# Kernel tuning notes

Hardware: AMD Instinct MI355X
Metric: run time of the kernel (lower is better)

## Reference

```python
import jax, jax.numpy as jnp
import numpy as np

LN_EPS = 1e-5
L1_EPS = 1e-12  # F.normalize clamp_min eps


def _layernorm(h, g, b):
    mu = h.mean(-1, keepdims=True)
    var = ((h - mu) ** 2).mean(-1, keepdims=True)
    return (h - mu) * jax.lax.rsqrt(var + LN_EPS) * g + b


def _graph(x, wq_w, wq_b, wk_w, wk_b, gcn_w, ln_g, ln_b):
    # x: [..., n, d]
    qx = x @ wq_w.T + wq_b
    kx = x @ wk_w.T + wk_b
    dot = jnp.einsum('...nd,...md->...nm', qx, kx)
    sq = dot * dot
    adj = sq / jnp.maximum(sq.sum(-1, keepdims=True), L1_EPS)  # L1-normalized rows
    for i in range(gcn_w.shape[0]):
        h = adj @ (x @ gcn_w[i])
        x = jax.nn.relu(_layernorm(h, ln_g[i], ln_b[i]))
    return x.mean(-2)  # mean over nodes -> [..., d]


def setup_inputs() -> dict:
    key = jax.random.key(0)
    ks = jax.random.split(key, 12)
    N, FR, B, NF = 16, 32, 50, 768
    L, NC = 2, 400
    s = 1.0 / np.sqrt(NF)
    inp = {
        'feats': jax.random.normal(ks[0], (N, FR, B, NF), jnp.float32),
        'feat_global_single': jax.random.normal(ks[1], (N, NF), jnp.float32),
        'feat_single_previous': jax.random.normal(ks[2], (N, NF), jnp.float32),
        'wq_w': jax.random.normal(ks[3], (NF, NF), jnp.float32) * s,
        'wq_b': jnp.zeros((NF,), jnp.float32),
        'wk_w': jax.random.normal(ks[4], (NF, NF), jnp.float32) * s,
        'wk_b': jnp.zeros((NF,), jnp.float32),
        'gcn_w': jax.random.normal(ks[5], (L, NF, NF), jnp.float32) * s,
        'ln_g': jnp.ones((L, NF), jnp.float32),
        'ln_b': jnp.zeros((L, NF), jnp.float32),
        'fc1_w': jax.random.normal(ks[6], (NF, 2 * NF), jnp.float32) / np.sqrt(2 * NF),
        'fc1_b': jnp.zeros((NF,), jnp.float32),
        'fc2_w': jax.random.normal(ks[7], (NC, NF), jnp.float32) * s,
        'fc2_b': jnp.zeros((NC,), jnp.float32),
        't_c': 0,
    }
    return inp


def reference(feats, feat_global_single, feat_single_previous,
              wq_w, wq_b, wk_w, wk_b, gcn_w, ln_g, ln_b,
              fc1_w, fc1_b, fc2_w, fc2_b, t_c):
    N, FR, B, NF = feats.shape
    x = feats.reshape(N * FR, B, NF)
    # object-level graph (shared weights)
    x = _graph(x, wq_w, wq_b, wk_w, wk_b, gcn_w, ln_g, ln_b)  # [N*FR, NF]
    x = x.reshape(N, FR, NF)
    # frame-level graph (same shared weights)
    x = _graph(x, wq_w, wq_b, wk_w, wk_b, gcn_w, ln_g, ln_b)  # [N, NF]
    y = jnp.concatenate([x, feat_global_single], axis=-1)      # [N, 2*NF]
    # ClassifierSimple (dropout = identity in eval)
    h = jax.nn.relu(y @ fc1_w.T + fc1_b)
    logits = h @ fc2_w.T + fc2_b
    return (logits, y)
```

## Files before the change

kernel.cpp:

```cpp
#include <hip/hip_runtime.h>
#include <hip/hip_bf16.h>

typedef unsigned short u16;
typedef unsigned int   u32;
typedef __attribute__((ext_vector_type(8))) short short8;
typedef __attribute__((ext_vector_type(4))) float float4v;

__device__ __forceinline__ float bf2f(u16 u){ union{u32 i; float f;} c; c.i = ((u32)u) << 16; return c.f; }
__device__ __forceinline__ float bflo(u32 u){ union{u32 i; float f;} c; c.i = u << 16; return c.f; }
__device__ __forceinline__ float bfhi(u32 u){ union{u32 i; float f;} c; c.i = u & 0xFFFF0000u; return c.f; }
__device__ __forceinline__ u16 f2bf(float f){
  union{float f; u32 i;} c; c.f = f; u32 x = c.i;
  return (u16)((x + 0x7FFFu + ((x >> 16) & 1u)) >> 16);
}
__device__ __forceinline__ u32 pack2(float a, float b){
  union { __hip_bfloat162 h; u32 u; } c;
  c.h = __float22bfloat162_rn(float2{a, b});
  return c.u;
}

__device__ __forceinline__ void async16(const void* g, void* l){
  __builtin_amdgcn_global_load_lds((const __attribute__((address_space(1))) void*)g,
                                   (__attribute__((address_space(3))) void*)l, 16, 0, 0);
}

__global__ void __launch_bounds__(256) conv_bf16(const float* __restrict__ src, u16* __restrict__ dst, int n8)
{
  int t = blockIdx.x * 256 + threadIdx.x;
  int stride = gridDim.x * 256;
  for (int i = t; i < n8; i += stride) {
    float4 a = ((const float4*)src)[2 * i];
    float4 b = ((const float4*)src)[2 * i + 1];
    uint4 o = { pack2(a.x, a.y), pack2(a.z, a.w), pack2(b.x, b.y), pack2(b.z, b.w) };
    ((uint4*)dst)[i] = o;
  }
}

__global__ void prep_qkw(const float* __restrict__ wq, const float* __restrict__ wk,
                         const float* __restrict__ wqb, const float* __restrict__ wkb,
                         u16* __restrict__ QHB, float* __restrict__ biasQH)
{
  int t = blockIdx.x * 256 + threadIdx.x;
  int stride = gridDim.x * 256;
  for (int i = t; i < 294912; i += stride) {
    float4 v = (i < 147456) ? ((const float4*)wq)[i] : ((const float4*)wk)[i - 147456];
    ushort4 o; o.x = f2bf(v.x); o.y = f2bf(v.y); o.z = f2bf(v.z); o.w = f2bf(v.w);
    ((ushort4*)QHB)[i] = o;
  }
  if (t < 768) biasQH[t] = wqb[t];
  else if (t < 1536) biasQH[t] = wkb[t - 768];
  else if (t < 2304) biasQH[t] = 0.f;
}

__global__ void prep_gcnT(const float* __restrict__ gcn, u16* __restrict__ QHB, u16* __restrict__ gcnT1)
{
  __shared__ float tile[32][33];
  int l = blockIdx.z;
  int d0 = blockIdx.y * 32, o0 = blockIdx.x * 32;
  int tx = threadIdx.x, ty = threadIdx.y;
  const float* src = gcn + (size_t)l * 589824;
  u16* dst = (l == 0) ? (QHB + (size_t)1536 * 768) : gcnT1;
  for (int i = 0; i < 32; i += 8) tile[ty + i][tx] = src[(size_t)(d0 + ty + i) * 768 + o0 + tx];
  __syncthreads();
  for (int i = 0; i < 32; i += 8) dst[(size_t)(o0 + ty + i) * 768 + d0 + tx] = f2bf(tile[tx][ty + i]);
}

__global__ void __launch_bounds__(256) gemm_bt(const u16* __restrict__ A, const u16* __restrict__ Bw,
                                               const float* __restrict__ bias, u16* __restrict__ C,
                                               int M, int N, int K)
{
  __shared__ __attribute__((aligned(16))) u16 As[128 * 64];
  __shared__ __attribute__((aligned(16))) u16 Bs[128 * 64];
  int tid = threadIdx.x, lane = tid & 63, wid = tid >> 6;
  int wm = wid >> 1, wn = wid & 1;
  size_t m0 = (size_t)blockIdx.x * 128, n0 = (size_t)blockIdx.y * 128;

  float4v acc[4][4];
  for (int r = 0; r < 4; r++) for (int c = 0; c < 4; c++) acc[r][c] = (float4v){0.f, 0.f, 0.f, 0.f};

  int srow8  = lane >> 3;
  int schunk = (lane & 7) ^ srow8;
  const u16* gA[4]; const u16* gB[4];
  u16* lA[4]; u16* lB[4];
#pragma unroll
  for (int j = 0; j < 4; j++) {
    int r = 32 * wid + 8 * j + srow8;
    gA[j] = A  + (m0 + r) * (size_t)K + schunk * 8;
    gB[j] = Bw + (n0 + r) * (size_t)K + schunk * 8;
    lA[j] = &As[(32 * wid + 8 * j) * 64];
    lB[j] = &Bs[(32 * wid + 8 * j) * 64];
  }

  int l15 = lane & 15, quad = lane >> 4;
  int s0 = quad ^ (l15 & 7);

  for (int kt = 0; kt < K; kt += 64) {
#pragma unroll
    for (int j = 0; j < 4; j++) {
      async16(gA[j] + kt, lA[j]);
      async16(gB[j] + kt, lB[j]);
    }
    __syncthreads();
#pragma unroll
    for (int ks = 0; ks < 2; ks++) {
      int so = (s0 ^ (ks << 2)) * 8;
      short8 af[4], bfr[4];
#pragma unroll
      for (int r = 0; r < 4; r++) af[r]  = *(const short8*)&As[(wm * 64 + r * 16 + l15) * 64 + so];
#pragma unroll
      for (int c = 0; c < 4; c++) bfr[c] = *(const short8*)&Bs[(wn * 64 + c * 16 + l15) * 64 + so];
#pragma unroll
      for (int r = 0; r < 4; r++)
#pragma unroll
        for (int c = 0; c < 4; c++)
          acc[r][c] = __builtin_amdgcn_mfma_f32_16x16x32_bf16(af[r], bfr[c], acc[r][c], 0, 0, 0);
    }
    __syncthreads();
  }

  int quad4 = quad * 4;
  for (int c = 0; c < 4; c++) {
    int n = (int)n0 + wn * 64 + c * 16 + l15;
    float bv = bias ? bias[n] : 0.f;
    for (int r = 0; r < 4; r++) {
      size_t mbase = m0 + wm * 64 + r * 16 + quad4;
      for (int t = 0; t < 4; t++)
        C[(mbase + t) * (size_t)N + n] = f2bf(acc[r][c][t] + bv);
    }
  }
}


template<int NP>
__global__ void __launch_bounds__(512) fused_l1(const u16* __restrict__ QH,
                                                const float* __restrict__ lng, const float* __restrict__ lnb,
                                                u16* __restrict__ adjG, u16* __restrict__ X, int n)
{
  constexpr int ST = 72;
  constexpr int TPW = (NP == 64) ? 2 : 1;
  __shared__ __attribute__((aligned(16))) u16 adjb[NP * ST];
  __shared__ __attribute__((aligned(16))) u16 HT[2][64 * ST];
  __shared__ float rsum[NP];
  __shared__ float stats[NP][2];
  __shared__ float bc[NP][2];
  __shared__ float lg[768], lb[768];

  int g = blockIdx.x;
  int tid = threadIdx.x, lane = tid & 63, w = tid >> 6;
  int l15 = lane & 15, quad = lane >> 4;

  for (int i = tid; i < 768; i += 512) { lg[i] = lng[i]; lb[i] = lnb[i]; }
  if (tid < NP) { rsum[tid] = 0.f; stats[tid][0] = 0.f; stats[tid][1] = 0.f; }
  __syncthreads();

  int mt, nt0; bool s_act;
  if (NP == 64) { mt = w & 3; nt0 = (w >> 2) * 2; s_act = true; }
  else          { mt = w & 1; nt0 = w >> 1;       s_act = (w < 4); }

  int rowA = mt * 16 + l15;
  bool aok = rowA < n;
  const u16* pA  = QH + ((size_t)g * n + rowA) * 2304 + quad * 8;
  int rowB0 = (nt0) * 16 + l15, rowB1 = (nt0 + TPW - 1) * 16 + l15;
  bool b0ok = rowB0 < n, b1ok = rowB1 < n;
  const u16* pB0 = QH + ((size_t)g * n + rowB0) * 2304 + 768 + quad * 8;
  const u16* pB1 = QH + ((size_t)g * n + rowB1) * 2304 + 768 + quad * 8;

  float4v sacc[TPW];
  for (int j = 0; j < TPW; j++) sacc[j] = (float4v){0.f, 0.f, 0.f, 0.f};

  if (s_act) {
    for (int kt = 0; kt < 768; kt += 32) {
      uint4 av = {0,0,0,0}, bv0 = {0,0,0,0}, bv1 = {0,0,0,0};
      if (aok)  av  = *(const uint4*)(pA + kt);
      if (b0ok) bv0 = *(const uint4*)(pB0 + kt);
      if (TPW == 2 && b1ok) bv1 = *(const uint4*)(pB1 + kt);
      short8 a = *(short8*)&av;
      sacc[0] = __builtin_amdgcn_mfma_f32_16x16x32_bf16(a, *(short8*)&bv0, sacc[0], 0, 0, 0);
      if (TPW == 2)
        sacc[1] = __builtin_amdgcn_mfma_f32_16x16x32_bf16(a, *(short8*)&bv1, sacc[1], 0, 0, 0);
    }
    for (int t = 0; t < 4; t++) {
      float s = 0.f;
      for (int j = 0; j < TPW; j++) { float v = sacc[j][t]; s += v * v; }
      s += __shfl_xor(s, 1); s += __shfl_xor(s, 2); s += __shfl_xor(s, 4); s += __shfl_xor(s, 8);
      if (l15 == 0) atomicAdd(&rsum[mt * 16 + quad * 4 + t], s);
    }
  }
  __syncthreads();
  if (tid < NP) rsum[tid] = 1.0f / fmaxf(rsum[tid], 1e-12f);
  __syncthreads();
  if (s_act) {
    u16* gadj = adjG + (size_t)g * NP * NP;
    for (int j = 0; j < TPW; j++)
      for (int t = 0; t < 4; t++) {
        int row = mt * 16 + quad * 4 + t, col = (nt0 + j) * 16 + l15;
        float v = sacc[j][t];
        u16 b = f2bf(v * v * rsum[row]);
        adjb[row * ST + col] = b;
        gadj[row * NP + col] = b;
      }
  }
  __syncthreads();

  int m2, nt20;
  if (NP == 64) { m2 = w & 3; nt20 = (w >> 2) * 2; }
  else          { m2 = w & 1; nt20 = w >> 1; }

  float4v xacc[12][TPW];
#pragma unroll
  for (int ch = 0; ch < 12; ch++) for (int j = 0; j < TPW; j++) xacc[ch][j] = (float4v){0.f,0.f,0.f,0.f};

  int hj  = tid & (NP - 1);
  int hseg= (NP == 64) ? w : ((tid >> 5) & 7);
  bool hact = (NP == 64) ? true : (tid < NP * 8);
  const u16* hbase = QH + ((size_t)g * n + hj) * 2304 + 1536 + hseg * 8;

  uint4 hcur = {0,0,0,0};
  if (hact && hj < n) hcur = *(const uint4*)(hbase);

#pragma unroll
  for (int ch = 0; ch < 12; ch++) {
    uint4 hnext = {0,0,0,0};
    if (ch < 11 && hact && hj < n) hnext = *(const uint4*)(hbase + (ch + 1) * 64);
    u16* htb = HT[ch & 1];
    if (hact) {
      const u16* ep = (const u16*)&hcur;
      for (int i = 0; i < 8; i++) htb[(hseg * 8 + i) * ST + hj] = ep[i];
    }
    __syncthreads();
    for (int k = 0; k < NP / 32; k++) {
      short8 a = *(const short8*)&adjb[(m2 * 16 + l15) * ST + k * 32 + quad * 8];
      for (int j = 0; j < TPW; j++) {
        short8 b = *(const short8*)&htb[((nt20 + j) * 16 + l15) * ST + k * 32 + quad * 8];
        xacc[ch][j] = __builtin_amdgcn_mfma_f32_16x16x32_bf16(a, b, xacc[ch][j], 0, 0, 0);
      }
    }
    hcur = hnext;
  }

  float ssum[4] = {0,0,0,0}, ssq[4] = {0,0,0,0};
#pragma unroll
  for (int ch = 0; ch < 12; ch++)
    for (int j = 0; j < TPW; j++)
      for (int t = 0; t < 4; t++) { float v = xacc[ch][j][t]; ssum[t] += v; ssq[t] += v * v; }
  for (int m = 1; m <= 8; m <<= 1)
    for (int t = 0; t < 4; t++) { ssum[t] += __shfl_xor(ssum[t], m); ssq[t] += __shfl_xor(ssq[t], m); }
  if (l15 == 0)
    for (int t = 0; t < 4; t++) {
      atomicAdd(&stats[m2 * 16 + quad * 4 + t][0], ssum[t]);
      atomicAdd(&stats[m2 * 16 + quad * 4 + t][1], ssq[t]);
    }
  __syncthreads();
  if (tid < NP) {
    float mu = stats[tid][0] * (1.f / 768.f);
    float var = stats[tid][1] * (1.f / 768.f) - mu * mu;
    bc[tid][0] = mu; bc[tid][1] = rsqrtf(fmaxf(var, 0.f) + 1e-5f);
  }
  __syncthreads();

#pragma unroll
  for (int ch = 0; ch < 12; ch++)
    for (int j = 0; j < TPW; j++)
      for (int t = 0; t < 4; t++) {
        int row = m2 * 16 + quad * 4 + t;
        if (row < n) {
          int d = ch * 64 + (nt20 + j) * 16 + l15;
          float v = fmaxf((xacc[ch][j][t] - bc[row][0]) * bc[row][1] * lg[d] + lb[d], 0.f);
          X[((size_t)g * n + row) * 768 + d] = f2bf(v);
        }
      }
}

template<int NP>
__global__ void __launch_bounds__(512) fused_l2(const u16* __restrict__ adjG, const u16* __restrict__ H,
                                                const float* __restrict__ lng, const float* __restrict__ lnb,
                                                u16* __restrict__ Xmean, int n, float inv)
{
  constexpr int ST = 72;
  constexpr int TPW = (NP == 64) ? 2 : 1;
  __shared__ __attribute__((aligned(16))) u16 adjb[NP * ST];
  __shared__ __attribute__((aligned(16))) u16 HT[2][64 * ST];
  __shared__ float stats[NP][2];
  __shared__ float bc[NP][2];
  __shared__ float colsum[768];
  __shared__ float lg[768], lb[768];

  int g = blockIdx.x;
  int tid = threadIdx.x, lane = tid & 63, w = tid >> 6;
  int l15 = lane & 15, quad = lane >> 4;

  for (int i = tid; i < 768; i += 512) { lg[i] = lng[i]; lb[i] = lnb[i]; colsum[i] = 0.f; }
  if (tid < NP) { stats[tid][0] = 0.f; stats[tid][1] = 0.f; }
  if (tid * 8 < NP * NP) {
    int row = (tid * 8) / NP, c0 = (tid * 8) % NP;
    uint4 v = *(const uint4*)(adjG + (size_t)g * NP * NP + row * NP + c0);
    *(uint4*)&adjb[row * ST + c0] = v;
  }

  int m2, nt20;
  if (NP == 64) { m2 = w & 3; nt20 = (w >> 2) * 2; }
  else          { m2 = w & 1; nt20 = w >> 1; }

  float4v xacc[12][TPW];
#pragma unroll
  for (int ch = 0; ch < 12; ch++) for (int j = 0; j < TPW; j++) xacc[ch][j] = (float4v){0.f,0.f,0.f,0.f};

  int hj  = tid & (NP - 1);
  int hseg= (NP == 64) ? w : ((tid >> 5) & 7);
  bool hact = (NP == 64) ? true : (tid < NP * 8);
  const u16* hbase = H + ((size_t)g * n + hj) * 768 + hseg * 8;

  uint4 hcur = {0,0,0,0};
  if (hact && hj < n) hcur = *(const uint4*)(hbase);

  __syncthreads();

#pragma unroll
  for (int ch = 0; ch < 12; ch++) {
    uint4 hnext = {0,0,0,0};
    if (ch < 11 && hact && hj < n) hnext = *(const uint4*)(hbase + (ch + 1) * 64);
    u16* htb = HT[ch & 1];
    if (hact) {
      const u16* ep = (const u16*)&hcur;
      for (int i = 0; i < 8; i++) htb[(hseg * 8 + i) * ST + hj] = ep[i];
    }
    __syncthreads();
    for (int k = 0; k < NP / 32; k++) {
      short8 a = *(const short8*)&adjb[(m2 * 16 + l15) * ST + k * 32 + quad * 8];
      for (int j = 0; j < TPW; j++) {
        short8 b = *(const short8*)&htb[((nt20 + j) * 16 + l15) * ST + k * 32 + quad * 8];
        xacc[ch][j] = __builtin_amdgcn_mfma_f32_16x16x32_bf16(a, b, xacc[ch][j], 0, 0, 0);
      }
    }
    hcur = hnext;
  }

  float ssum[4] = {0,0,0,0}, ssq[4] = {0,0,0,0};
#pragma unroll
  for (int ch = 0; ch < 12; ch++)
    for (int j = 0; j < TPW; j++)
      for (int t = 0; t < 4; t++) { float v = xacc[ch][j][t]; ssum[t] += v; ssq[t] += v * v; }
  for (int m = 1; m <= 8; m <<= 1)
    for (int t = 0; t < 4; t++) { ssum[t] += __shfl_xor(ssum[t], m); ssq[t] += __shfl_xor(ssq[t], m); }
  if (l15 == 0)
    for (int t = 0; t < 4; t++) {
      atomicAdd(&stats[m2 * 16 + quad * 4 + t][0], ssum[t]);
      atomicAdd(&stats[m2 * 16 + quad * 4 + t][1], ssq[t]);
    }
  __syncthreads();
  if (tid < NP) {
    float mu = stats[tid][0] * (1.f / 768.f);
    float var = stats[tid][1] * (1.f / 768.f) - mu * mu;
    bc[tid][0] = mu; bc[tid][1] = rsqrtf(fmaxf(var, 0.f) + 1e-5f);
  }
  __syncthreads();

#pragma unroll
  for (int ch = 0; ch < 12; ch++)
    for (int j = 0; j < TPW; j++)
      for (int t = 0; t < 4; t++) {
        int row = m2 * 16 + quad * 4 + t;
        int d = ch * 64 + (nt20 + j) * 16 + l15;
        float v = fmaxf((xacc[ch][j][t] - bc[row][0]) * bc[row][1] * lg[d] + lb[d], 0.f);
        float vm = (row < n) ? v : 0.f;
        vm += __shfl_xor(vm, 16);
        vm += __shfl_xor(vm, 32);
        if (quad == 0) atomicAdd(&colsum[d], vm);
      }
  __syncthreads();
  if (tid < 384)
    ((u32*)Xmean)[(size_t)g * 384 + tid] = pack2(colsum[tid * 2] * inv, colsum[tid * 2 + 1] * inv);
}

__global__ void __launch_bounds__(384) concat_y(const u16* __restrict__ Xm,
                                                const float* __restrict__ fgs, float* __restrict__ yout)
{
  int b = blockIdx.x, tid = threadIdx.x;
  u32 u = ((const u32*)Xm)[(size_t)b * 384 + tid];
  int d0 = tid * 2;
  yout[(size_t)b * 1536 + d0]     = bflo(u);
  yout[(size_t)b * 1536 + d0 + 1] = bfhi(u);
  yout[(size_t)b * 1536 + 768 + d0]     = fgs[(size_t)b * 768 + d0];
  yout[(size_t)b * 1536 + 768 + d0 + 1] = fgs[(size_t)b * 768 + d0 + 1];
}

__global__ void __launch_bounds__(256) fc1_relu(const float* __restrict__ yout,
                                                const float* __restrict__ fc1w, const float* __restrict__ fc1b,
                                                float* __restrict__ h)
{
  int o = blockIdx.x * 4 + (threadIdx.x >> 6);
  int lane = threadIdx.x & 63;
  float acc[16];
  for (int b = 0; b < 16; b++) acc[b] = 0.f;
  const float4* wr = (const float4*)(fc1w + (size_t)o * 1536);
  for (int k4 = lane; k4 < 384; k4 += 64) {
    float4 wv = wr[k4];
    for (int b = 0; b < 16; b++) {
      float4 yv = ((const float4*)(yout + (size_t)b * 1536))[k4];
      acc[b] += wv.x * yv.x + wv.y * yv.y + wv.z * yv.z + wv.w * yv.w;
    }
  }
  for (int m = 1; m <= 32; m <<= 1)
    for (int b = 0; b < 16; b++) acc[b] += __shfl_xor(acc[b], m);
  if (lane < 16) h[(size_t)lane * 768 + o] = fmaxf(acc[lane] + fc1b[o], 0.f);
}

__global__ void __launch_bounds__(256) fc2_out(const float* __restrict__ h,
                                               const float* __restrict__ fc2w, const float* __restrict__ fc2b,
                                               float* __restrict__ logits)
{
  int o = blockIdx.x * 4 + (threadIdx.x >> 6);
  int lane = threadIdx.x & 63;
  float acc[16];
  for (int b = 0; b < 16; b++) acc[b] = 0.f;
  const float4* wr = (const float4*)(fc2w + (size_t)o * 768);
  for (int k4 = lane; k4 < 192; k4 += 64) {
    float4 wv = wr[k4];
    for (int b = 0; b < 16; b++) {
      float4 hv = ((const float4*)(h + (size_t)b * 768))[k4];
      acc[b] += wv.x * hv.x + wv.y * hv.y + wv.z * hv.z + wv.w * hv.w;
    }
  }
  for (int m = 1; m <= 32; m <<= 1)
    for (int b = 0; b < 16; b++) acc[b] += __shfl_xor(acc[b], m);
  if (lane < 16) logits[(size_t)lane * 400 + o] = acc[lane] + fc2b[o];
}

extern "C" void kernel_launch(void* const* d_in, const int* in_sizes, int n_in,
                              void* d_out, int out_size, void* d_ws, size_t ws_size,
                              hipStream_t stream) {
  const float* feats = (const float*)d_in[0];
  const float* fgs   = (const float*)d_in[1];
  const float* wq_w  = (const float*)d_in[3];
  const float* wq_b  = (const float*)d_in[4];
  const float* wk_w  = (const float*)d_in[5];
  const float* wk_b  = (const float*)d_in[6];
  const float* gcn_w = (const float*)d_in[7];
  const float* ln_g  = (const float*)d_in[8];
  const float* ln_b  = (const float*)d_in[9];
  const float* fc1_w = (const float*)d_in[10];
  const float* fc1_b = (const float*)d_in[11];
  const float* fc2_w = (const float*)d_in[12];
  const float* fc2_b = (const float*)d_in[13];
  float* out  = (float*)d_out;
  float* yout = out + 16 * 400;

  char* ws = (char*)d_ws;
  size_t off = 0;
  auto alloc = [&](size_t b){ size_t r = off; off = (off + b + 255) & ~(size_t)255; return r; };
  u16*  QHB    = (u16*) (ws + alloc((size_t)2304 * 768 * 2));
  u16*  gcnT1  = (u16*) (ws + alloc((size_t)768 * 768 * 2));
  float* biasQH= (float*)(ws + alloc((size_t)2304 * 4));
  u16*  Abf    = (u16*) (ws + alloc((size_t)25600 * 768 * 2));
  u16*  Xf     = (u16*) (ws + alloc((size_t)512 * 768 * 2));
  u16*  QHf    = (u16*) (ws + alloc((size_t)512 * 2304 * 2));
  u16*  X1f    = (u16*) (ws + alloc((size_t)512 * 768 * 2));
  u16*  H2f    = (u16*) (ws + alloc((size_t)512 * 768 * 2));
  u16*  adjFb  = (u16*) (ws + alloc((size_t)16 * 32 * 32 * 2));
  u16*  Xm     = (u16*) (ws + alloc((size_t)16 * 768 * 2));
  float* hbuf  = (float*)(ws + alloc((size_t)16 * 768 * 4));
  size_t base = off;

  auto need = [&](int GC){
    size_t R = (size_t)GC * 50;
    return base + R * 2304 * 2 + 512 + R * 768 * 2 + 512 + (size_t)GC * 64 * 64 * 2 + 512;
  };
  int GC = 64;
  if (need(512) <= ws_size) GC = 512;
  else if (need(256) <= ws_size) GC = 256;
  else if (need(128) <= ws_size) GC = 128;
  int R = GC * 50;
  size_t off2 = base;
  auto alloc2 = [&](size_t b){ size_t r = off2; off2 = (off2 + b + 255) & ~(size_t)255; return r; };
  u16* QHc   = (u16*)(ws + alloc2((size_t)R * 2304 * 2));
  u16* X1c   = (u16*)(ws + alloc2((size_t)R * 768 * 2));
  u16* adjGc = (u16*)(ws + alloc2((size_t)GC * 64 * 64 * 2));
  u16* H2c   = QHc;

  conv_bf16<<<2048, 256, 0, stream>>>(feats, Abf, 25600 * 768 / 8);
  prep_qkw<<<288, 256, 0, stream>>>(wq_w, wk_w, wq_b, wk_b, QHB, biasQH);
  prep_gcnT<<<dim3(24, 24, 2), dim3(32, 8), 0, stream>>>(gcn_w, QHB, gcnT1);

  int nchunks = 512 / GC;
  for (int c = 0; c < nchunks; c++) {
    const u16* fc = Abf + (size_t)c * GC * 50 * 768;
    gemm_bt<<<dim3(R / 128, 18), 256, 0, stream>>>(fc, QHB, biasQH, QHc, R, 2304, 768);
    fused_l1<64><<<GC, 512, 0, stream>>>(QHc, ln_g, ln_b, adjGc, X1c, 50);
    gemm_bt<<<dim3(R / 128, 6), 256, 0, stream>>>(X1c, gcnT1, nullptr, H2c, R, 768, 768);
    fused_l2<64><<<GC, 512, 0, stream>>>(adjGc, H2c, ln_g + 768, ln_b + 768,
                                         Xf + (size_t)c * GC * 768, 50, 1.f / 50.f);
  }

  gemm_bt<<<dim3(4, 18), 256, 0, stream>>>(Xf, QHB, biasQH, QHf, 512, 2304, 768);
  fused_l1<32><<<16, 512, 0, stream>>>(QHf, ln_g, ln_b, adjFb, X1f, 32);
  gemm_bt<<<dim3(4, 6), 256, 0, stream>>>(X1f, gcnT1, nullptr, H2f, 512, 768, 768);
  fused_l2<32><<<16, 512, 0, stream>>>(adjFb, H2f, ln_g + 768, ln_b + 768, Xm, 32, 1.f / 32.f);

  concat_y<<<16, 384, 0, stream>>>(Xm, fgs, yout);
  fc1_relu<<<192, 256, 0, stream>>>(yout, fc1_w, fc1_b, hbuf);
  fc2_out<<<100, 256, 0, stream>>>(hbuf, fc2_w, fc2_b, out);
}
```

Measured before the change: 509.6 us.

## Double-buffer bf16 GEMM with 256x256 tiles and 512-thread blocks

Reworks the main GEMM kernel to use 256x256 output tiles with 8 waves per block, and double-buffers the LDS tiles so the next K-slice's async global-to-LDS loads overlap the current slice's MFMAs. It waits with explicit vmcnt and raw barriers, and raises wave priority around the MFMA sequence. It adds M-bounds clamping and store guards so row counts that are not multiples of 256 work. The cost is 128KB of LDS per block, which limits occupancy, and fewer blocks for the small frame-level GEMMs.

```diff
diff --git a/kernel.cpp b/kernel.cpp
--- a/kernel.cpp
+++ b/kernel.cpp
@@ -65,67 +65,90 @@
   for (int i = 0; i < 32; i += 8) dst[(size_t)(o0 + ty + i) * 768 + d0 + tx] = f2bf(tile[tx][ty + i]);
 }
 
-__global__ void __launch_bounds__(256) gemm_bt(const u16* __restrict__ A, const u16* __restrict__ Bw,
-                                               const float* __restrict__ bias, u16* __restrict__ C,
-                                               int M, int N, int K)
-{
-  __shared__ __attribute__((aligned(16))) u16 As[128 * 64];
-  __shared__ __attribute__((aligned(16))) u16 Bs[128 * 64];
+__global__ void __launch_bounds__(512, 2) gemm_bt(const u16* __restrict__ A, const u16* __restrict__ Bw,
+                                                  const float* __restrict__ bias, u16* __restrict__ C,
+                                                  int M, int N, int K)
+{
+  __shared__ __attribute__((aligned(16))) u16 As[2][256 * 64];
+  __shared__ __attribute__((aligned(16))) u16 Bs[2][256 * 64];
   int tid = threadIdx.x, lane = tid & 63, wid = tid >> 6;
-  int wm = wid >> 1, wn = wid & 1;
-  size_t m0 = (size_t)blockIdx.x * 128, n0 = (size_t)blockIdx.y * 128;
-
-  float4v acc[4][4];
-  for (int r = 0; r < 4; r++) for (int c = 0; c < 4; c++) acc[r][c] = (float4v){0.f, 0.f, 0.f, 0.f};
+  int wm = wid >> 2, wn = wid & 3;
+  size_t m0 = (size_t)blockIdx.x * 256, n0 = (size_t)blockIdx.y * 256;
+
+  float4v acc[8][4];
+#pragma unroll
+  for (int r = 0; r < 8; r++)
+#pragma unroll
+    for (int c = 0; c < 4; c++) acc[r][c] = (float4v){0.f, 0.f, 0.f, 0.f};
 
   int srow8  = lane >> 3;
   int schunk = (lane & 7) ^ srow8;
-  const u16* gA[4]; const u16* gB[4];
-  u16* lA[4]; u16* lB[4];
+  const u16* gA[4]; const u16* gB[4]; int ldsO[4];
 #pragma unroll
   for (int j = 0; j < 4; j++) {
     int r = 32 * wid + 8 * j + srow8;
-    gA[j] = A  + (m0 + r) * (size_t)K + schunk * 8;
+    size_t rA = m0 + r; if (rA >= (size_t)M) rA = M - 1;
+    gA[j] = A  + rA * (size_t)K + schunk * 8;
     gB[j] = Bw + (n0 + r) * (size_t)K + schunk * 8;
-    lA[j] = &As[(32 * wid + 8 * j) * 64];
-    lB[j] = &Bs[(32 * wid + 8 * j) * 64];
+    ldsO[j] = (32 * wid + 8 * j) * 64;
   }
 
   int l15 = lane & 15, quad = lane >> 4;
-  int s0 = quad ^ (l15 & 7);
-
-  for (int kt = 0; kt < K; kt += 64) {
-#pragma unroll
-    for (int j = 0; j < 4; j++) {
-      async16(gA[j] + kt, lA[j]);
-      async16(gB[j] + kt, lB[j]);
-    }
-    __syncthreads();
+  int l7 = l15 & 7;
+  int nk = K >> 6;
+
+#pragma unroll
+  for (int j = 0; j < 4; j++) {
+    async16(gA[j], &As[0][ldsO[j]]);
+    async16(gB[j], &Bs[0][ldsO[j]]);
+  }
+
+  for (int t = 0; t < nk; ++t) {
+    int cur = t & 1, nxt = cur ^ 1;
+    if (t + 1 < nk) {
+      int kt = (t + 1) << 6;
+#pragma unroll
+      for (int j = 0; j < 4; j++) {
+        async16(gA[j] + kt, &As[nxt][ldsO[j]]);
+        async16(gB[j] + kt, &Bs[nxt][ldsO[j]]);
+      }
+      asm volatile("s_waitcnt vmcnt(8)" ::: "memory");
+    } else {
+      asm volatile("s_waitcnt vmcnt(0)" ::: "memory");
+    }
+    __builtin_amdgcn_s_barrier();
+    __builtin_amdgcn_sched_barrier(0);
+
 #pragma unroll
     for (int ks = 0; ks < 2; ks++) {
-      int so = (s0 ^ (ks << 2)) * 8;
-      short8 af[4], bfr[4];
-#pragma unroll
-      for (int r = 0; r < 4; r++) af[r]  = *(const short8*)&As[(wm * 64 + r * 16 + l15) * 64 + so];
-#pragma unroll
-      for (int c = 0; c < 4; c++) bfr[c] = *(const short8*)&Bs[(wn * 64 + c * 16 + l15) * 64 + so];
-#pragma unroll
-      for (int r = 0; r < 4; r++)
+      int so = ((quad ^ l7) ^ (ks << 2)) * 8;
+      short8 bfr[4];
+#pragma unroll
+      for (int c = 0; c < 4; c++)
+        bfr[c] = *(const short8*)&Bs[cur][(wn * 64 + c * 16 + l15) * 64 + so];
+      __builtin_amdgcn_s_setprio(1);
+#pragma unroll
+      for (int r = 0; r < 8; r++) {
+        short8 a = *(const short8*)&As[cur][(wm * 128 + r * 16 + l15) * 64 + so];
 #pragma unroll
         for (int c = 0; c < 4; c++)
-          acc[r][c] = __builtin_amdgcn_mfma_f32_16x16x32_bf16(af[r], bfr[c], acc[r][c], 0, 0, 0);
-    }
-    __syncthreads();
+          acc[r][c] = __builtin_amdgcn_mfma_f32_16x16x32_bf16(a, bfr[c], acc[r][c], 0, 0, 0);
+      }
+      __builtin_amdgcn_s_setprio(0);
+    }
+    __builtin_amdgcn_sched_barrier(0);
+    __builtin_amdgcn_s_barrier();
   }
 
   int quad4 = quad * 4;
   for (int c = 0; c < 4; c++) {
     int n = (int)n0 + wn * 64 + c * 16 + l15;
     float bv = bias ? bias[n] : 0.f;
-    for (int r = 0; r < 4; r++) {
-      size_t mbase = m0 + wm * 64 + r * 16 + quad4;
+    for (int r = 0; r < 8; r++) {
+      size_t mbase = m0 + wm * 128 + r * 16 + quad4;
       for (int t = 0; t < 4; t++)
-        C[(mbase + t) * (size_t)N + n] = f2bf(acc[r][c][t] + bv);
+        if (mbase + t < (size_t)M)
+          C[(mbase + t) * (size_t)N + n] = f2bf(acc[r][c][t] + bv);
     }
   }
 }
@@ -484,16 +507,17 @@
   int nchunks = 512 / GC;
   for (int c = 0; c < nchunks; c++) {
     const u16* fc = Abf + (size_t)c * GC * 50 * 768;
-    gemm_bt<<<dim3(R / 128, 18), 256, 0, stream>>>(fc, QHB, biasQH, QHc, R, 2304, 768);
+    int mt = (R + 255) / 256;
+    gemm_bt<<<dim3(mt, 9), 512, 0, stream>>>(fc, QHB, biasQH, QHc, R, 2304, 768);
     fused_l1<64><<<GC, 512, 0, stream>>>(QHc, ln_g, ln_b, adjGc, X1c, 50);
-    gemm_bt<<<dim3(R / 128, 6), 256, 0, stream>>>(X1c, gcnT1, nullptr, H2c, R, 768, 768);
+    gemm_bt<<<dim3(mt, 3), 512, 0, stream>>>(X1c, gcnT1, nullptr, H2c, R, 768, 768);
     fused_l2<64><<<GC, 512, 0, stream>>>(adjGc, H2c, ln_g + 768, ln_b + 768,
                                          Xf + (size_t)c * GC * 768, 50, 1.f / 50.f);
   }
 
-  gemm_bt<<<dim3(4, 18), 256, 0, stream>>>(Xf, QHB, biasQH, QHf, 512, 2304, 768);
+  gemm_bt<<<dim3(2, 9), 512, 0, stream>>>(Xf, QHB, biasQH, QHf, 512, 2304, 768);
   fused_l1<32><<<16, 512, 0, stream>>>(QHf, ln_g, ln_b, adjFb, X1f, 32);
-  gemm_bt<<<dim3(4, 6), 256, 0, stream>>>(X1f, gcnT1, nullptr, H2f, 512, 768, 768);
+  gemm_bt<<<dim3(2, 3), 512, 0, stream>>>(X1f, gcnT1, nullptr, H2f, 512, 768, 768);
   fused_l2<32><<<16, 512, 0, stream>>>(adjFb, H2f, ln_g + 768, ln_b + 768, Xm, 32, 1.f / 32.f);
 
   concat_y<<<16, 384, 0, stream>>>(Xm, fgs, yout);
```

After: 669.7 us. +31.4%, slower.

## Fold Wq and Wk into a single bilinear matrix to shrink projection GEMM

Applied to the files above, without the earlier changes.

Rewrites the attention score q·k as x Wq^T Wk x^T plus rank-one bias terms. The combined 768x768 matrix is precomputed by a small GEMM, and the bias contributions come from per-row dot products (p, q) computed in a new kernel. The big per-chunk projection GEMM now produces 1536 columns instead of 2304, and the score GEMM reads the raw bf16 input rows directly. The cost is extra prep kernels, a separate pass over the inputs for the bias scalars, and bf16 rounding of the fused weight product, which may shift accuracy.

```diff
diff --git a/kernel.cpp b/kernel.cpp
--- a/kernel.cpp
+++ b/kernel.cpp
@@ -36,20 +36,14 @@
   }
 }
 
-__global__ void prep_qkw(const float* __restrict__ wq, const float* __restrict__ wk,
-                         const float* __restrict__ wqb, const float* __restrict__ wkb,
-                         u16* __restrict__ QHB, float* __restrict__ biasQH)
-{
-  int t = blockIdx.x * 256 + threadIdx.x;
-  int stride = gridDim.x * 256;
-  for (int i = t; i < 294912; i += stride) {
-    float4 v = (i < 147456) ? ((const float4*)wq)[i] : ((const float4*)wk)[i - 147456];
-    ushort4 o; o.x = f2bf(v.x); o.y = f2bf(v.y); o.z = f2bf(v.z); o.w = f2bf(v.w);
-    ((ushort4*)QHB)[i] = o;
-  }
-  if (t < 768) biasQH[t] = wqb[t];
-  else if (t < 1536) biasQH[t] = wkb[t - 768];
-  else if (t < 2304) biasQH[t] = 0.f;
+__global__ void transpose_bf16(const float* __restrict__ src, u16* __restrict__ dst)
+{
+  __shared__ float tile[32][33];
+  int r0 = blockIdx.y * 32, c0 = blockIdx.x * 32;
+  int tx = threadIdx.x, ty = threadIdx.y;
+  for (int i = 0; i < 32; i += 8) tile[ty + i][tx] = src[(size_t)(r0 + ty + i) * 768 + c0 + tx];
+  __syncthreads();
+  for (int i = 0; i < 32; i += 8) dst[(size_t)(c0 + ty + i) * 768 + r0 + tx] = f2bf(tile[tx][ty + i]);
 }
 
 __global__ void prep_gcnT(const float* __restrict__ gcn, u16* __restrict__ QHB, u16* __restrict__ gcnT1)
@@ -59,10 +53,56 @@
   int d0 = blockIdx.y * 32, o0 = blockIdx.x * 32;
   int tx = threadIdx.x, ty = threadIdx.y;
   const float* src = gcn + (size_t)l * 589824;
-  u16* dst = (l == 0) ? (QHB + (size_t)1536 * 768) : gcnT1;
+  u16* dst = (l == 0) ? (QHB + (size_t)768 * 768) : gcnT1;
   for (int i = 0; i < 32; i += 8) tile[ty + i][tx] = src[(size_t)(d0 + ty + i) * 768 + o0 + tx];
   __syncthreads();
   for (int i = 0; i < 32; i += 8) dst[(size_t)(o0 + ty + i) * 768 + d0 + tx] = f2bf(tile[tx][ty + i]);
+}
+
+__global__ void __launch_bounds__(256) prep_uv(const float* __restrict__ wq, const float* __restrict__ wk,
+                                               const float* __restrict__ wqb, const float* __restrict__ wkb,
+                                               float* __restrict__ uv, float* __restrict__ cbuf)
+{
+  if (blockIdx.x < 6) {
+    int t = blockIdx.x * 256 + threadIdx.x;
+    if (t < 768) {
+      float a = 0.f;
+      for (int o = 0; o < 768; o++) a += wq[(size_t)o * 768 + t] * wkb[o];
+      uv[t] = a;
+    } else {
+      int d = t - 768;
+      float a = 0.f;
+      for (int o = 0; o < 768; o++) a += wk[(size_t)o * 768 + d] * wqb[o];
+      uv[t] = a;
+    }
+  } else {
+    __shared__ float red[256];
+    float a = 0.f;
+    for (int o = threadIdx.x; o < 768; o += 256) a += wqb[o] * wkb[o];
+    red[threadIdx.x] = a; __syncthreads();
+    if (threadIdx.x == 0) { float s = 0.f; for (int i = 0; i < 256; i++) s += red[i]; cbuf[0] = s; }
+  }
+}
+
+__global__ void __launch_bounds__(256) row_pq(const u16* __restrict__ X, const float* __restrict__ uv,
+                                              const float* __restrict__ cbuf, float* __restrict__ p,
+                                              float* __restrict__ q, int Mrows)
+{
+  __shared__ float us[768], vs[768];
+  int tid = threadIdx.x, lane = tid & 63, w = tid >> 6;
+  for (int i = tid; i < 768; i += 256) { us[i] = uv[i]; vs[i] = uv[768 + i]; }
+  __syncthreads();
+  int row = blockIdx.x * 4 + w;
+  if (row >= Mrows) return;
+  const u16* xr = X + (size_t)row * 768;
+  float ap = 0.f, aq = 0.f;
+  for (int k = 0; k < 12; k++) {
+    int d = k * 64 + lane;
+    float x = bf2f(xr[d]);
+    ap += x * us[d]; aq += x * vs[d];
+  }
+  for (int m = 1; m <= 32; m <<= 1) { ap += __shfl_xor(ap, m); aq += __shfl_xor(aq, m); }
+  if (lane == 0) { p[row] = ap + cbuf[0]; q[row] = aq; }
 }
 
 __global__ void __launch_bounds__(256) gemm_bt(const u16* __restrict__ A, const u16* __restrict__ Bw,
@@ -132,7 +172,8 @@
 
 
 template<int NP>
-__global__ void __launch_bounds__(512) fused_l1(const u16* __restrict__ QH,
+__global__ void __launch_bounds__(512) fused_l1(const u16* __restrict__ TH, const u16* __restrict__ AR,
+                                                const float* __restrict__ pb, const float* __restrict__ qb,
                                                 const float* __restrict__ lng, const float* __restrict__ lnb,
                                                 u16* __restrict__ adjG, u16* __restrict__ X, int n)
 {
@@ -143,6 +184,7 @@
   __shared__ float rsum[NP];
   __shared__ float stats[NP][2];
   __shared__ float bc[NP][2];
+  __shared__ float ps[NP], qs[NP];
   __shared__ float lg[768], lb[768];
 
   int g = blockIdx.x;
@@ -150,7 +192,11 @@
   int l15 = lane & 15, quad = lane >> 4;
 
   for (int i = tid; i < 768; i += 512) { lg[i] = lng[i]; lb[i] = lnb[i]; }
-  if (tid < NP) { rsum[tid] = 0.f; stats[tid][0] = 0.f; stats[tid][1] = 0.f; }
+  if (tid < NP) {
+    rsum[tid] = 0.f; stats[tid][0] = 0.f; stats[tid][1] = 0.f;
+    ps[tid] = (tid < n) ? pb[(size_t)g * n + tid] : 0.f;
+    qs[tid] = (tid < n) ? qb[(size_t)g * n + tid] : 0.f;
+  }
   __syncthreads();
 
   int mt, nt0; bool s_act;
@@ -159,11 +205,11 @@
 
   int rowA = mt * 16 + l15;
   bool aok = rowA < n;
-  const u16* pA  = QH + ((size_t)g * n + rowA) * 2304 + quad * 8;
+  const u16* tA  = TH + ((size_t)g * n + rowA) * 1536 + quad * 8;
   int rowB0 = (nt0) * 16 + l15, rowB1 = (nt0 + TPW - 1) * 16 + l15;
   bool b0ok = rowB0 < n, b1ok = rowB1 < n;
-  const u16* pB0 = QH + ((size_t)g * n + rowB0) * 2304 + 768 + quad * 8;
-  const u16* pB1 = QH + ((size_t)g * n + rowB1) * 2304 + 768 + quad * 8;
+  const u16* pB0 = AR + ((size_t)g * n + rowB0) * 768 + quad * 8;
+  const u16* pB1 = AR + ((size_t)g * n + rowB1) * 768 + quad * 8;
 
   float4v sacc[TPW];
   for (int j = 0; j < TPW; j++) sacc[j] = (float4v){0.f, 0.f, 0.f, 0.f};
@@ -171,13 +217,21 @@
   if (s_act) {
     for (int kt = 0; kt < 768; kt += 32) {
       uint4 av = {0,0,0,0}, bv0 = {0,0,0,0}, bv1 = {0,0,0,0};
-      if (aok)  av  = *(const uint4*)(pA + kt);
+      if (aok)  av  = *(const uint4*)(tA + kt);
       if (b0ok) bv0 = *(const uint4*)(pB0 + kt);
       if (TPW == 2 && b1ok) bv1 = *(const uint4*)(pB1 + kt);
       short8 a = *(short8*)&av;
       sacc[0] = __builtin_amdgcn_mfma_f32_16x16x32_bf16(a, *(short8*)&bv0, sacc[0], 0, 0, 0);
       if (TPW == 2)
         sacc[1] = __builtin_amdgcn_mfma_f32_16x16x32_bf16(a, *(short8*)&bv1, sacc[1], 0, 0, 0);
+    }
+    for (int j = 0; j < TPW; j++) {
+      int col = (nt0 + j) * 16 + l15;
+      bool cok = col < n;
+      for (int t = 0; t < 4; t++) {
+        int row = mt * 16 + quad * 4 + t;
+        sacc[j][t] = cok ? (sacc[j][t] + ps[row] + qs[col]) : 0.f;
+      }
     }
     for (int t = 0; t < 4; t++) {
       float s = 0.f;
@@ -213,7 +267,7 @@
   int hj  = tid & (NP - 1);
   int hseg= (NP == 64) ? w : ((tid >> 5) & 7);
   bool hact = (NP == 64) ? true : (tid < NP * 8);
-  const u16* hbase = QH + ((size_t)g * n + hj) * 2304 + 1536 + hseg * 8;
+  const u16* hbase = TH + ((size_t)g * n + hj) * 1536 + 768 + hseg * 8;
 
   uint4 hcur = {0,0,0,0};
   if (hact && hj < n) hcur = *(const uint4*)(hbase);
@@ -448,12 +502,19 @@
   char* ws = (char*)d_ws;
   size_t off = 0;
   auto alloc = [&](size_t b){ size_t r = off; off = (off + b + 255) & ~(size_t)255; return r; };
-  u16*  QHB    = (u16*) (ws + alloc((size_t)2304 * 768 * 2));
+  u16*  QHB    = (u16*) (ws + alloc((size_t)1536 * 768 * 2));
   u16*  gcnT1  = (u16*) (ws + alloc((size_t)768 * 768 * 2));
-  float* biasQH= (float*)(ws + alloc((size_t)2304 * 4));
+  u16*  WqT    = (u16*) (ws + alloc((size_t)768 * 768 * 2));
+  u16*  WkT    = (u16*) (ws + alloc((size_t)768 * 768 * 2));
+  float* uv    = (float*)(ws + alloc((size_t)1536 * 4));
+  float* cbuf  = (float*)(ws + alloc((size_t)4));
   u16*  Abf    = (u16*) (ws + alloc((size_t)25600 * 768 * 2));
+  float* pObj  = (float*)(ws + alloc((size_t)25600 * 4));
+  float* qObj  = (float*)(ws + alloc((size_t)25600 * 4));
+  float* pF    = (float*)(ws + alloc((size_t)512 * 4));
+  float* qF    = (float*)(ws + alloc((size_t)512 * 4));
   u16*  Xf     = (u16*) (ws + alloc((size_t)512 * 768 * 2));
-  u16*  QHf    = (u16*) (ws + alloc((size_t)512 * 2304 * 2));
+  u16*  QHf    = (u16*) (ws + alloc((size_t)512 * 1536 * 2));
   u16*  X1f    = (u16*) (ws + alloc((size_t)512 * 768 * 2));
   u16*  H2f    = (u16*) (ws + alloc((size_t)512 * 768 * 2));
   u16*  adjFb  = (u16*) (ws + alloc((size_t)16 * 32 * 32 * 2));
@@ -463,7 +524,7 @@
 
   auto need = [&](int GC){
     size_t R = (size_t)GC * 50;
-    return base + R * 2304 * 2 + 512 + R * 768 * 2 + 512 + (size_t)GC * 64 * 64 * 2 + 512;
+    return base + R * 1536 * 2 + 512 + R * 768 * 2 + 512 + (size_t)GC * 64 * 64 * 2 + 512;
   };
   int GC = 64;
   if (need(512) <= ws_size) GC = 512;
@@ -472,27 +533,33 @@
   int R = GC * 50;
   size_t off2 = base;
   auto alloc2 = [&](size_t b){ size_t r = off2; off2 = (off2 + b + 255) & ~(size_t)255; return r; };
-  u16* QHc   = (u16*)(ws + alloc2((size_t)R * 2304 * 2));
+  u16* QHc   = (u16*)(ws + alloc2((size_t)R * 1536 * 2));
   u16* X1c   = (u16*)(ws + alloc2((size_t)R * 768 * 2));
   u16* adjGc = (u16*)(ws + alloc2((size_t)GC * 64 * 64 * 2));
   u16* H2c   = QHc;
 
+  transpose_bf16<<<dim3(24, 24), dim3(32, 8), 0, stream>>>(wq_w, WqT);
+  transpose_bf16<<<dim3(24, 24), dim3(32, 8), 0, stream>>>(wk_w, WkT);
+  prep_uv<<<7, 256, 0, stream>>>(wq_w, wk_w, wq_b, wk_b, uv, cbuf);
+  gemm_bt<<<dim3(6, 6), 256, 0, stream>>>(WkT, WqT, nullptr, QHB, 768, 768, 768);
+  prep_gcnT<<<dim3(24, 24, 2), dim3(32, 8), 0, stream>>>(gcn_w, QHB, gcnT1);
   conv_bf16<<<2048, 256, 0, stream>>>(feats, Abf, 25600 * 768 / 8);
-  prep_qkw<<<288, 256, 0, stream>>>(wq_w, wk_w, wq_b, wk_b, QHB, biasQH);
-  prep_gcnT<<<dim3(24, 24, 2), dim3(32, 8), 0, stream>>>(gcn_w, QHB, gcnT1);
+  row_pq<<<6400, 256, 0, stream>>>(Abf, uv, cbuf, pObj, qObj, 25600);
 
   int nchunks = 512 / GC;
   for (int c = 0; c < nchunks; c++) {
     const u16* fc = Abf + (size_t)c * GC * 50 * 768;
-    gemm_bt<<<dim3(R / 128, 18), 256, 0, stream>>>(fc, QHB, biasQH, QHc, R, 2304, 768);
-    fused_l1<64><<<GC, 512, 0, stream>>>(QHc, ln_g, ln_b, adjGc, X1c, 50);
+    gemm_bt<<<dim3(R / 128, 12), 256, 0, stream>>>(fc, QHB, nullptr, QHc, R, 1536, 768);
+    fused_l1<64><<<GC, 512, 0, stream>>>(QHc, fc, pObj + (size_t)c * GC * 50, qObj + (size_t)c * GC * 50,
+                                         ln_g, ln_b, adjGc, X1c, 50);
     gemm_bt<<<dim3(R / 128, 6), 256, 0, stream>>>(X1c, gcnT1, nullptr, H2c, R, 768, 768);
     fused_l2<64><<<GC, 512, 0, stream>>>(adjGc, H2c, ln_g + 768, ln_b + 768,
                                          Xf + (size_t)c * GC * 768, 50, 1.f / 50.f);
   }
 
-  gemm_bt<<<dim3(4, 18), 256, 0, stream>>>(Xf, QHB, biasQH, QHf, 512, 2304, 768);
-  fused_l1<32><<<16, 512, 0, stream>>>(QHf, ln_g, ln_b, adjFb, X1f, 32);
+  row_pq<<<128, 256, 0, stream>>>(Xf, uv, cbuf, pF, qF, 512);
+  gemm_bt<<<dim3(4, 12), 256, 0, stream>>>(Xf, QHB, nullptr, QHf, 512, 1536, 768);
+  fused_l1<32><<<16, 512, 0, stream>>>(QHf, Xf, pF, qF, ln_g, ln_b, adjFb, X1f, 32);
   gemm_bt<<<dim3(4, 6), 256, 0, stream>>>(X1f, gcnT1, nullptr, H2f, 512, 768, 768);
   fused_l2<32><<<16, 512, 0, stream>>>(adjFb, H2f, ln_g + 768, ln_b + 768, Xm, 32, 1.f / 32.f);
 
```

New measurement: 553.0 us. 1.09x slower.
